# Optimization experiments

Measured on AMD Instinct MI355X. Metric: run time of the kernel, lower is better.

The kernel has to match this reference:

```python
import jax, jax.numpy as jnp
import numpy as np

B, T, C = 4, 2048, 1024
H = 16
D = C // H  # head_dim = 64


def setup_inputs() -> dict:
    key = jax.random.key(0)
    ks = jax.random.split(key, 9)
    s = 1.0 / np.sqrt(C)
    return {
        "x": jax.random.normal(ks[0], (B, T, C), dtype=jnp.float32),
        "wq": jax.random.uniform(ks[1], (C, C), jnp.float32, -s, s),
        "bq": jax.random.uniform(ks[2], (C,), jnp.float32, -s, s),
        "wk": jax.random.uniform(ks[3], (C, C), jnp.float32, -s, s),
        "bk": jax.random.uniform(ks[4], (C,), jnp.float32, -s, s),
        "wv": jax.random.uniform(ks[5], (C, C), jnp.float32, -s, s),
        "bv": jax.random.uniform(ks[6], (C,), jnp.float32, -s, s),
        "wo": jax.random.uniform(ks[7], (C, C), jnp.float32, -s, s),
        "bo": jax.random.uniform(ks[8], (C,), jnp.float32, -s, s),
    }


def reference(x, wq, bq, wk, bk, wv, bv, wo, bo):
    # Linear layers (torch convention: y = x @ W.T + b)
    q = x @ wq.T + bq  # [B,T,C]
    k = x @ wk.T + bk
    v = x @ wv.T + bv
    # split heads -> [B,H,T,D]
    q = q.reshape(B, T, H, D).transpose(0, 2, 1, 3)
    k = k.reshape(B, T, H, D).transpose(0, 2, 1, 3)
    v = v.reshape(B, T, H, D).transpose(0, 2, 1, 3)
    scores = jnp.einsum('bhqd,bhkd->bhqk', q, k) / jnp.sqrt(jnp.float32(D))
    causal = jnp.tril(jnp.ones((T, T), dtype=bool))  # position i attends to j<=i
    scores = jnp.where(causal, scores, -jnp.inf)
    attn = jax.nn.softmax(scores, axis=-1)
    # dropout p=0.0 (eval / identity)
    out = jnp.einsum('bhqk,bhkd->bhqd', attn, v)  # [B,H,T,D]
    out = out.transpose(0, 2, 1, 3).reshape(B, T, C)
    return out @ wo.T + bo
```

## Files before the change

kernel.cpp:

```cpp
#include <hip/hip_runtime.h>
#include <stdint.h>

#define B_DIM 4
#define T_DIM 2048
#define C_DIM 1024
#define H_DIM 16
#define D_DIM 64
#define M_DIM (B_DIM * T_DIM)
#define QK_SCALE 0.18033688011112042f

typedef float f32x4 __attribute__((ext_vector_type(4)));
typedef float f32x16 __attribute__((ext_vector_type(16)));
typedef short bf16x8 __attribute__((ext_vector_type(8)));
typedef unsigned short u16;
typedef u16 u16x8 __attribute__((ext_vector_type(8)));

static __device__ __forceinline__ u16 f2b(float f) {
  uint32_t r;
  asm("v_cvt_pk_bf16_f32 %0, %1, %1" : "=v"(r) : "v"(f));
  return (u16)r;
}
static __device__ __forceinline__ uint32_t f2b2(float a, float b) {
  uint32_t r;
  asm("v_cvt_pk_bf16_f32 %0, %1, %2" : "=v"(r) : "v"(a), "v"(b));
  return r;
}
static __device__ __forceinline__ float xhalf_max(float x) {
  return fmaxf(x, __shfl_xor(x, 32, 64));
}
static __device__ __forceinline__ float xhalf_sum(float x) {
  return x + __shfl_xor(x, 32, 64);
}

static __device__ __forceinline__ void gl_lds16(const u16* g, u16* l) {
  __builtin_amdgcn_global_load_lds(
      (const __attribute__((address_space(1))) void*)g,
      (__attribute__((address_space(3))) void*)l, 16, 0, 0);
}

__global__ void k_cvt_all(const float* __restrict__ x,
                          const float* __restrict__ s0, const float* __restrict__ s1,
                          const float* __restrict__ s2, const float* __restrict__ s3,
                          u16* __restrict__ dx,
                          u16* __restrict__ d0, u16* __restrict__ d1,
                          u16* __restrict__ d2, u16* __restrict__ d3) {
  int i = blockIdx.x * blockDim.x + threadIdx.x;
  const float* s;
  u16* d;
  int j;
  if (i < (1 << 21)) {
    s = x; d = dx; j = i;
  } else {
    int k = i - (1 << 21);
    int seg = k >> 18;
    j = k & ((1 << 18) - 1);
    s = seg == 0 ? s0 : seg == 1 ? s1 : seg == 2 ? s2 : s3;
    d = seg == 0 ? d0 : seg == 1 ? d1 : seg == 2 ? d2 : d3;
  }
  float4 v = ((const float4*)s)[j];
  uint2 o;
  o.x = f2b2(v.x, v.y);
  o.y = f2b2(v.z, v.w);
  ((uint2*)d)[j] = o;
}

__global__ __launch_bounds__(256) void k_gemm_qkv(
    const u16* __restrict__ A,
    const u16* __restrict__ w0, const u16* __restrict__ w1, const u16* __restrict__ w2,
    const float* __restrict__ b0, const float* __restrict__ b1, const float* __restrict__ b2,
    u16* __restrict__ Qo, u16* __restrict__ Ko, u16* __restrict__ Vto) {
  __shared__ u16 As[128 * 32];
  __shared__ u16 Bs[128 * 32];
  const int tid = threadIdx.x;
  const int l = tid & 63;
  const int w = tid >> 6;
  const int wr = w >> 1, wc = w & 1;
  const int seg = blockIdx.x >> 3;
  const int brow = blockIdx.y * 128, bcol = (blockIdx.x & 7) * 128;
  const int lrow = l & 15, lk = l >> 4;
  const int K = C_DIM;

  const u16* Bw = seg == 0 ? w0 : seg == 1 ? w1 : w2;
  const float* bias = seg == 0 ? b0 : seg == 1 ? b1 : b2;
  const float scale = seg == 0 ? QK_SCALE : 1.f;

  f32x4 acc[4][4];
  for (int m = 0; m < 4; ++m)
    for (int n = 0; n < 4; ++n)
      acc[m][n] = (f32x4){0.f, 0.f, 0.f, 0.f};

  for (int kt = 0; kt < K; kt += 32) {
    __syncthreads();
    {
      int slot = tid;
      int r0 = slot >> 2, c0 = slot & 3;
      gl_lds16(A + (size_t)(brow + r0) * K + kt + c0 * 8, As + slot * 8);
      gl_lds16(Bw + (size_t)(bcol + r0) * K + kt + c0 * 8, Bs + slot * 8);
      int slot2 = slot + 256;
      int r1 = slot2 >> 2, c1 = slot2 & 3;
      gl_lds16(A + (size_t)(brow + r1) * K + kt + c1 * 8, As + slot2 * 8);
      gl_lds16(Bw + (size_t)(bcol + r1) * K + kt + c1 * 8, Bs + slot2 * 8);
    }
    asm volatile("s_waitcnt vmcnt(0)" ::: "memory");
    __syncthreads();

    bf16x8 af[4], bfr[4];
#pragma unroll
    for (int m = 0; m < 4; ++m)
      af[m] = *(const bf16x8*)(As + (wr * 64 + m * 16 + lrow) * 32 + lk * 8);
#pragma unroll
    for (int n = 0; n < 4; ++n)
      bfr[n] = *(const bf16x8*)(Bs + (wc * 64 + n * 16 + lrow) * 32 + lk * 8);
#pragma unroll
    for (int m = 0; m < 4; ++m) {
#pragma unroll
      for (int n = 0; n < 4; ++n)
        acc[m][n] = __builtin_amdgcn_mfma_f32_16x16x32_bf16(af[m], bfr[n], acc[m][n], 0, 0, 0);
    }
  }

#pragma unroll
  for (int m = 0; m < 4; ++m) {
    int rg0 = brow + wr * 64 + m * 16 + lk * 4;
    int bb = rg0 >> 11, tt0 = rg0 & (T_DIM - 1);
#pragma unroll
    for (int n = 0; n < 4; ++n) {
      int cg = bcol + wc * 64 + n * 16 + lrow;
      float bv = bias[cg];
      int hh = cg >> 6, dd = cg & 63;
      if (seg == 2) {
        float v0 = acc[m][n][0] + bv, v1 = acc[m][n][1] + bv;
        float v2 = acc[m][n][2] + bv, v3 = acc[m][n][3] + bv;
        uint2 pv;
        pv.x = f2b2(v0, v1);
        pv.y = f2b2(v2, v3);
        *(uint2*)(Vto + (((size_t)bb * H_DIM + hh) * D_DIM + dd) * T_DIM + tt0) = pv;
      } else {
        u16* Out = seg == 0 ? Qo : Ko;
#pragma unroll
        for (int i = 0; i < 4; ++i) {
          float val = (acc[m][n][i] + bv) * scale;
          Out[(((size_t)bb * H_DIM + hh) * T_DIM + tt0 + i) * D_DIM + dd] = f2b(val);
        }
      }
    }
  }
}

__global__ __launch_bounds__(256) void k_gemm_proj(
    const u16* __restrict__ A, const u16* __restrict__ Bw,
    const float* __restrict__ bias, float* __restrict__ Cout) {
  __shared__ u16 As[128 * 32];
  __shared__ u16 Bs[128 * 32];
  const int tid = threadIdx.x;
  const int l = tid & 63;
  const int w = tid >> 6;
  const int wr = w >> 1, wc = w & 1;
  const int brow = blockIdx.y * 128, bcol = blockIdx.x * 128;
  const int lrow = l & 15, lk = l >> 4;
  const int K = C_DIM, N = C_DIM;

  f32x4 acc[4][4];
  for (int m = 0; m < 4; ++m)
    for (int n = 0; n < 4; ++n)
      acc[m][n] = (f32x4){0.f, 0.f, 0.f, 0.f};

  for (int kt = 0; kt < K; kt += 32) {
    __syncthreads();
    {
      int slot = tid;
      int r0 = slot >> 2, c0 = slot & 3;
      gl_lds16(A + (size_t)(brow + r0) * K + kt + c0 * 8, As + slot * 8);
      gl_lds16(Bw + (size_t)(bcol + r0) * K + kt + c0 * 8, Bs + slot * 8);
      int slot2 = slot + 256;
      int r1 = slot2 >> 2, c1 = slot2 & 3;
      gl_lds16(A + (size_t)(brow + r1) * K + kt + c1 * 8, As + slot2 * 8);
      gl_lds16(Bw + (size_t)(bcol + r1) * K + kt + c1 * 8, Bs + slot2 * 8);
    }
    asm volatile("s_waitcnt vmcnt(0)" ::: "memory");
    __syncthreads();

    bf16x8 af[4], bfr[4];
#pragma unroll
    for (int m = 0; m < 4; ++m)
      af[m] = *(const bf16x8*)(As + (wr * 64 + m * 16 + lrow) * 32 + lk * 8);
#pragma unroll
    for (int n = 0; n < 4; ++n)
      bfr[n] = *(const bf16x8*)(Bs + (wc * 64 + n * 16 + lrow) * 32 + lk * 8);
#pragma unroll
    for (int m = 0; m < 4; ++m) {
#pragma unroll
      for (int n = 0; n < 4; ++n)
        acc[m][n] = __builtin_amdgcn_mfma_f32_16x16x32_bf16(af[m], bfr[n], acc[m][n], 0, 0, 0);
    }
  }

#pragma unroll
  for (int m = 0; m < 4; ++m) {
    int rg0 = brow + wr * 64 + m * 16 + lk * 4;
#pragma unroll
    for (int n = 0; n < 4; ++n) {
      int cg = bcol + wc * 64 + n * 16 + lrow;
      float bv = bias[cg];
#pragma unroll
      for (int i = 0; i < 4; ++i)
        Cout[(size_t)(rg0 + i) * N + cg] = acc[m][n][i] + bv;
    }
  }
}

__global__ __launch_bounds__(512) void k_attn(
    const u16* __restrict__ Q, const u16* __restrict__ Kg,
    const u16* __restrict__ Vt, u16* __restrict__ O) {
  __shared__ u16 Ks[2][128 * 64];
  __shared__ u16 Vs[2][64 * 128];

  const int tid = threadIdx.x;
  const int l = tid & 63;
  const int w = tid >> 6;
  const int id = blockIdx.x;
  int bh, qb;
  if (id < 256) { bh = id >> 2; qb = 7 - (id & 3); }
  else { bh = (id - 256) >> 2; qb = (id - 256) & 3; }
  const int q0 = qb * 256;
  const int ql = l & 31;
  const int hi = l >> 5;
  const int r0 = q0 + w * 32;
  const int qg = r0 + ql;

  const size_t qkbase = (size_t)bh * T_DIM * D_DIM;
  const size_t vtbase = (size_t)bh * D_DIM * T_DIM;

  const int sr = tid >> 3, sc = tid & 7;
  const int kcol = (sc ^ (sr & 7)) * 8;
  const int vr = tid >> 4, vc = tid & 15;
  const int vcol = (vc ^ (vr & 7)) * 8;

#define STAGE(buf, kt)                                                                    \
  {                                                                                       \
    gl_lds16(Kg + qkbase + (size_t)((kt) * 128 + sr) * D_DIM + kcol, Ks[buf] + tid * 8);  \
    gl_lds16(Kg + qkbase + (size_t)((kt) * 128 + 64 + sr) * D_DIM + kcol,                 \
             Ks[buf] + 4096 + tid * 8);                                                   \
    gl_lds16(Vt + vtbase + (size_t)vr * T_DIM + (kt) * 128 + vcol, Vs[buf] + tid * 8);    \
    gl_lds16(Vt + vtbase + (size_t)(vr + 32) * T_DIM + (kt) * 128 + vcol,                 \
             Vs[buf] + 4096 + tid * 8);                                                   \
  }

  bf16x8 qf[4];
#pragma unroll
  for (int kk = 0; kk < 4; ++kk)
    qf[kk] = *(const bf16x8*)(Q + qkbase + (size_t)qg * D_DIM + kk * 16 + hi * 8);

  f32x16 oacc[2];
#pragma unroll
  for (int dt = 0; dt < 2; ++dt)
#pragma unroll
    for (int r = 0; r < 16; ++r) oacc[dt][r] = 0.f;
  float m_run = -1e30f, l_run = 0.f;

  const int tdiag64 = r0 >> 6;
  const int nkt = (q0 >> 7) + 2;

  STAGE(0, 0);

  for (int kt = 0; kt < nkt; ++kt) {
    const int cur = kt & 1;
    if (kt + 1 < nkt) {
      STAGE(cur ^ 1, kt + 1);
      asm volatile("s_waitcnt vmcnt(4)" ::: "memory");
    } else {
      asm volatile("s_waitcnt vmcnt(0)" ::: "memory");
    }
    __syncthreads();

#pragma unroll
    for (int h2 = 0; h2 < 2; ++h2) {
      const int kt64 = kt * 2 + h2;
      if (kt64 <= tdiag64) {
        const u16* Kt = Ks[cur] + h2 * 4096;
        f32x16 s[2];
#pragma unroll
        for (int a = 0; a < 2; ++a)
#pragma unroll
          for (int r = 0; r < 16; ++r) s[a][r] = 0.f;

        __builtin_amdgcn_s_setprio(1);
#pragma unroll
        for (int kk = 0; kk < 4; ++kk) {
#pragma unroll
          for (int a = 0; a < 2; ++a) {
            int row = a * 32 + ql;
            int blk = (kk * 2 + hi) ^ (row & 7);
            bf16x8 kf = *(const bf16x8*)(Kt + row * 64 + blk * 8);
            s[a] = __builtin_amdgcn_mfma_f32_32x32x16_bf16(kf, qf[kk], s[a], 0, 0, 0);
          }
        }
        __builtin_amdgcn_s_setprio(0);

        if (kt64 == tdiag64) {
#pragma unroll
          for (int a = 0; a < 2; ++a) {
#pragma unroll
            for (int r = 0; r < 16; ++r) {
              int kv = kt64 * 64 + a * 32 + (r & 3) + 8 * (r >> 2) + 4 * hi;
              if (kv > qg) s[a][r] = -1e30f;
            }
          }
        }

        float t[16];
#pragma unroll
        for (int r = 0; r < 16; ++r) t[r] = fmaxf(s[0][r], s[1][r]);
#pragma unroll
        for (int r = 0; r < 8; ++r) t[r] = fmaxf(t[r], t[r + 8]);
#pragma unroll
        for (int r = 0; r < 4; ++r) t[r] = fmaxf(t[r], t[r + 4]);
        float pm = fmaxf(fmaxf(t[0], t[1]), fmaxf(t[2], t[3]));
        pm = xhalf_max(pm);

        if (__any(pm > m_run + 8.f)) {
          float mn = fmaxf(m_run, pm);
          float sc_ = exp2f(m_run - mn);
          m_run = mn;
          l_run *= sc_;
#pragma unroll
          for (int dt = 0; dt < 2; ++dt)
#pragma unroll
            for (int r = 0; r < 16; ++r) oacc[dt][r] *= sc_;
        }

        float rs0 = 0.f, rs1 = 0.f, rs2 = 0.f, rs3 = 0.f;
#pragma unroll
        for (int a = 0; a < 2; ++a) {
#pragma unroll
          for (int r = 0; r < 16; ++r) {
            float p = exp2f(s[a][r] - m_run);
            s[a][r] = p;
            if ((r & 3) == 0) rs0 += p;
            else if ((r & 3) == 1) rs1 += p;
            else if ((r & 3) == 2) rs2 += p;
            else rs3 += p;
          }
        }
        float rs = (rs0 + rs1) + (rs2 + rs3);
        l_run += xhalf_sum(rs);

#pragma unroll
        for (int kk = 0; kk < 4; ++kk) {
          const int a = kk >> 1;
          const int base = (kk & 1) * 8;
          union { uint32_t wd[4]; bf16x8 v; } pf;
#pragma unroll
          for (int i = 0; i < 2; ++i) {
            uint32_t Aw = f2b2(s[a][base + 2 * i], s[a][base + 2 * i + 1]);
            uint32_t Bw = f2b2(s[a][base + 4 + 2 * i], s[a][base + 5 + 2 * i]);
            uint32_t As_ = (uint32_t)__shfl_xor((int)Aw, 32, 64);
            uint32_t Bs_ = (uint32_t)__shfl_xor((int)Bw, 32, 64);
            pf.wd[i] = hi ? Bs_ : Aw;
            pf.wd[2 + i] = hi ? Bw : As_;
          }
          __builtin_amdgcn_s_setprio(1);
#pragma unroll
          for (int dt = 0; dt < 2; ++dt) {
            int row = dt * 32 + ql;
            int chunk = (h2 * 8) + ((kk * 2 + hi) ^ (row & 7));
            bf16x8 vf = *(const bf16x8*)(Vs[cur] + row * 128 + chunk * 8);
            oacc[dt] = __builtin_amdgcn_mfma_f32_32x32x16_bf16(vf, pf.v, oacc[dt], 0, 0, 0);
          }
          __builtin_amdgcn_s_setprio(0);
        }
      }
    }
    __syncthreads();
  }

  const int bb = bh >> 4, hh = bh & 15;
  const float inv = 1.f / l_run;
  u16* orow = O + ((size_t)bb * T_DIM + qg) * C_DIM + hh * D_DIM;
#pragma unroll
  for (int dt = 0; dt < 2; ++dt) {
#pragma unroll
    for (int g = 0; g < 4; ++g) {
      uint2 val;
      val.x = f2b2(oacc[dt][g * 4 + 0] * inv, oacc[dt][g * 4 + 1] * inv);
      val.y = f2b2(oacc[dt][g * 4 + 2] * inv, oacc[dt][g * 4 + 3] * inv);
      *(uint2*)(orow + dt * 32 + g * 8 + 4 * hi) = val;
    }
  }
}

extern "C" void kernel_launch(void* const* d_in, const int* in_sizes, int n_in,
                              void* d_out, int out_size, void* d_ws, size_t ws_size,
                              hipStream_t stream) {
  (void)in_sizes; (void)n_in; (void)out_size; (void)ws_size;
  const float* x  = (const float*)d_in[0];
  const float* wq = (const float*)d_in[1];
  const float* bq = (const float*)d_in[2];
  const float* wk = (const float*)d_in[3];
  const float* bk = (const float*)d_in[4];
  const float* wv = (const float*)d_in[5];
  const float* bv = (const float*)d_in[6];
  const float* wo = (const float*)d_in[7];
  const float* bo = (const float*)d_in[8];
  float* out = (float*)d_out;

  u16* xb  = (u16*)d_ws;
  u16* wqb = xb + (size_t)M_DIM * C_DIM;
  u16* wkb = wqb + (size_t)C_DIM * C_DIM;
  u16* wvb = wkb + (size_t)C_DIM * C_DIM;
  u16* wob = wvb + (size_t)C_DIM * C_DIM;
  u16* Qb  = wob + (size_t)C_DIM * C_DIM;
  u16* Kb  = Qb + (size_t)M_DIM * C_DIM;
  u16* Vtb = Kb + (size_t)M_DIM * C_DIM;
  u16* Ob  = Vtb + (size_t)M_DIM * C_DIM;

  k_cvt_all<<<12288, 256, 0, stream>>>(x, wq, wk, wv, wo, xb, wqb, wkb, wvb, wob);

  k_gemm_qkv<<<dim3(24, M_DIM / 128), 256, 0, stream>>>(
      xb, wqb, wkb, wvb, bq, bk, bv, Qb, Kb, Vtb);

  k_attn<<<512, 512, 0, stream>>>(Qb, Kb, Vtb, Ob);
  k_gemm_proj<<<dim3(C_DIM / 128, M_DIM / 128), 256, 0, stream>>>(Ob, wob, bo, out);
}
```

Measured before the change: 196.1 us.

## Process 128-key tiles per softmax step and remap blocks to XCDs by head

The attention loop now computes scores for a full 128-key tile (four 32x32 MFMA accumulators) before one online-softmax update, instead of two 64-key halves each with its own max and rescale. This halves the reduction, rescale-check and cross-lane shuffle overhead per key and gives the MFMA stream longer runs. It costs more registers for the score tile and wastes work on fully masked 64-key halves at the diagonal. Block-to-(head, query-block) mapping is also changed so blocks of the same head land on the same XCD, aiming for better L2 reuse of K/V.

```diff
diff --git a/kernel.cpp b/kernel.cpp
--- a/kernel.cpp
+++ b/kernel.cpp
@@ -219,9 +219,13 @@
   const int l = tid & 63;
   const int w = tid >> 6;
   const int id = blockIdx.x;
-  int bh, qb;
-  if (id < 256) { bh = id >> 2; qb = 7 - (id & 3); }
-  else { bh = (id - 256) >> 2; qb = (id - 256) & 3; }
+  const int xcd = id & 7;
+  const int half = id >> 8;
+  const int idh = id & 255;
+  const int slot = (idh >> 3) & 7;
+  const int j = idh >> 6;
+  const int bh = xcd * 8 + slot;
+  const int qb = half ? j : 7 - j;
   const int q0 = qb * 256;
   const int ql = l & 31;
   const int hi = l >> 5;
@@ -258,7 +262,7 @@
     for (int r = 0; r < 16; ++r) oacc[dt][r] = 0.f;
   float m_run = -1e30f, l_run = 0.f;
 
-  const int tdiag64 = r0 >> 6;
+  const int tdx = r0 >> 7;
   const int nkt = (q0 >> 7) + 2;
 
   STAGE(0, 0);
@@ -273,87 +277,91 @@
     }
     __syncthreads();
 
-#pragma unroll
-    for (int h2 = 0; h2 < 2; ++h2) {
-      const int kt64 = kt * 2 + h2;
-      if (kt64 <= tdiag64) {
+    if (kt <= tdx) {
+      f32x16 s4[4];
+#pragma unroll
+      for (int a = 0; a < 4; ++a)
+#pragma unroll
+        for (int r = 0; r < 16; ++r) s4[a][r] = 0.f;
+
+      __builtin_amdgcn_s_setprio(1);
+#pragma unroll
+      for (int h2 = 0; h2 < 2; ++h2) {
         const u16* Kt = Ks[cur] + h2 * 4096;
-        f32x16 s[2];
-#pragma unroll
-        for (int a = 0; a < 2; ++a)
-#pragma unroll
-          for (int r = 0; r < 16; ++r) s[a][r] = 0.f;
-
-        __builtin_amdgcn_s_setprio(1);
 #pragma unroll
         for (int kk = 0; kk < 4; ++kk) {
 #pragma unroll
-          for (int a = 0; a < 2; ++a) {
-            int row = a * 32 + ql;
+          for (int aa = 0; aa < 2; ++aa) {
+            int row = aa * 32 + ql;
             int blk = (kk * 2 + hi) ^ (row & 7);
             bf16x8 kf = *(const bf16x8*)(Kt + row * 64 + blk * 8);
-            s[a] = __builtin_amdgcn_mfma_f32_32x32x16_bf16(kf, qf[kk], s[a], 0, 0, 0);
+            s4[h2 * 2 + aa] =
+                __builtin_amdgcn_mfma_f32_32x32x16_bf16(kf, qf[kk], s4[h2 * 2 + aa], 0, 0, 0);
           }
         }
-        __builtin_amdgcn_s_setprio(0);
-
-        if (kt64 == tdiag64) {
-#pragma unroll
-          for (int a = 0; a < 2; ++a) {
-#pragma unroll
-            for (int r = 0; r < 16; ++r) {
-              int kv = kt64 * 64 + a * 32 + (r & 3) + 8 * (r >> 2) + 4 * hi;
-              if (kv > qg) s[a][r] = -1e30f;
-            }
+      }
+      __builtin_amdgcn_s_setprio(0);
+
+      if (kt == tdx) {
+#pragma unroll
+        for (int a = 0; a < 4; ++a) {
+#pragma unroll
+          for (int r = 0; r < 16; ++r) {
+            int kv = kt * 128 + a * 32 + (r & 3) + 8 * (r >> 2) + 4 * hi;
+            if (kv > qg) s4[a][r] = -1e30f;
           }
         }
-
-        float t[16];
-#pragma unroll
-        for (int r = 0; r < 16; ++r) t[r] = fmaxf(s[0][r], s[1][r]);
-#pragma unroll
-        for (int r = 0; r < 8; ++r) t[r] = fmaxf(t[r], t[r + 8]);
-#pragma unroll
-        for (int r = 0; r < 4; ++r) t[r] = fmaxf(t[r], t[r + 4]);
-        float pm = fmaxf(fmaxf(t[0], t[1]), fmaxf(t[2], t[3]));
-        pm = xhalf_max(pm);
-
-        if (__any(pm > m_run + 8.f)) {
-          float mn = fmaxf(m_run, pm);
-          float sc_ = exp2f(m_run - mn);
-          m_run = mn;
-          l_run *= sc_;
-#pragma unroll
-          for (int dt = 0; dt < 2; ++dt)
-#pragma unroll
-            for (int r = 0; r < 16; ++r) oacc[dt][r] *= sc_;
+      }
+
+      float t16[16];
+#pragma unroll
+      for (int r = 0; r < 16; ++r)
+        t16[r] = fmaxf(fmaxf(s4[0][r], s4[1][r]), fmaxf(s4[2][r], s4[3][r]));
+#pragma unroll
+      for (int r = 0; r < 8; ++r) t16[r] = fmaxf(t16[r], t16[r + 8]);
+#pragma unroll
+      for (int r = 0; r < 4; ++r) t16[r] = fmaxf(t16[r], t16[r + 4]);
+      float pm = fmaxf(fmaxf(t16[0], t16[1]), fmaxf(t16[2], t16[3]));
+      pm = xhalf_max(pm);
+
+      if (__any(pm > m_run + 8.f)) {
+        float mn = fmaxf(m_run, pm);
+        float sc_ = exp2f(m_run - mn);
+        m_run = mn;
+        l_run *= sc_;
+#pragma unroll
+        for (int dt = 0; dt < 2; ++dt)
+#pragma unroll
+          for (int r = 0; r < 16; ++r) oacc[dt][r] *= sc_;
+      }
+
+      float rs0 = 0.f, rs1 = 0.f, rs2 = 0.f, rs3 = 0.f;
+#pragma unroll
+      for (int a = 0; a < 4; ++a) {
+#pragma unroll
+        for (int r = 0; r < 16; ++r) {
+          float p = exp2f(s4[a][r] - m_run);
+          s4[a][r] = p;
+          if ((r & 3) == 0) rs0 += p;
+          else if ((r & 3) == 1) rs1 += p;
+          else if ((r & 3) == 2) rs2 += p;
+          else rs3 += p;
         }
-
-        float rs0 = 0.f, rs1 = 0.f, rs2 = 0.f, rs3 = 0.f;
-#pragma unroll
-        for (int a = 0; a < 2; ++a) {
-#pragma unroll
-          for (int r = 0; r < 16; ++r) {
-            float p = exp2f(s[a][r] - m_run);
-            s[a][r] = p;
-            if ((r & 3) == 0) rs0 += p;
-            else if ((r & 3) == 1) rs1 += p;
-            else if ((r & 3) == 2) rs2 += p;
-            else rs3 += p;
-          }
-        }
-        float rs = (rs0 + rs1) + (rs2 + rs3);
-        l_run += xhalf_sum(rs);
-
+      }
+      float rs = (rs0 + rs1) + (rs2 + rs3);
+      l_run += xhalf_sum(rs);
+
+#pragma unroll
+      for (int h2 = 0; h2 < 2; ++h2) {
 #pragma unroll
         for (int kk = 0; kk < 4; ++kk) {
-          const int a = kk >> 1;
+          const int a = h2 * 2 + (kk >> 1);
           const int base = (kk & 1) * 8;
           union { uint32_t wd[4]; bf16x8 v; } pf;
 #pragma unroll
           for (int i = 0; i < 2; ++i) {
-            uint32_t Aw = f2b2(s[a][base + 2 * i], s[a][base + 2 * i + 1]);
-            uint32_t Bw = f2b2(s[a][base + 4 + 2 * i], s[a][base + 5 + 2 * i]);
+            uint32_t Aw = f2b2(s4[a][base + 2 * i], s4[a][base + 2 * i + 1]);
+            uint32_t Bw = f2b2(s4[a][base + 4 + 2 * i], s4[a][base + 5 + 2 * i]);
             uint32_t As_ = (uint32_t)__shfl_xor((int)Aw, 32, 64);
             uint32_t Bs_ = (uint32_t)__shfl_xor((int)Bw, 32, 64);
             pf.wd[i] = hi ? Bs_ : Aw;
```

New measurement: 216.9 us. +10.6%, slower.
